# Optimization experiments

Hardware: AMD Instinct MI355X
Metric: run time of the kernel (lower is better)

The kernel has to match this reference:

```python
import jax, jax.numpy as jnp
import numpy as np
import math

B, T, C = 2, 2048, 1024
H = 16
D = C // H            # head_dim = 64
E = 4                 # num_experts
TOP_K = 1
EPS_RMS = 1.1920929e-07  # torch fp32 machine eps (F.rms_norm default)


def rms_norm(x):
    # F.rms_norm over last dim, no learned weight
    ms = jnp.mean(jnp.square(x), axis=-1, keepdims=True)
    return x * jax.lax.rsqrt(ms + EPS_RMS)


def rotary_cos_sin(seq_len, dim):
    inv_freq = 1.0 / (10000.0 ** (jnp.arange(0, dim, 2, dtype=jnp.float32) / dim))
    t = jnp.arange(seq_len, dtype=jnp.float32)
    freqs = jnp.outer(t, inv_freq)                 # [T, D/2]
    return jnp.cos(freqs)[None, :, None, :], jnp.sin(freqs)[None, :, None, :]


def apply_rotary(x, cos, sin):
    d = x.shape[-1] // 2
    x1, x2 = x[..., :d], x[..., d:]
    return jnp.concatenate([x1 * cos + x2 * sin, -x1 * sin + x2 * cos], axis=-1)


def setup_inputs() -> dict:
    key = jax.random.key(0)
    ks = jax.random.split(key, 8)
    s_attn = 1.0 / math.sqrt(C)
    s_fc = 1.0 / math.sqrt(C)
    s_pr = 1.0 / math.sqrt(4 * C)
    return {
        "x": jax.random.normal(ks[0], (B, T, C), jnp.float32),
        "Wq": jax.random.normal(ks[1], (C, C), jnp.float32) * s_attn,
        "Wk": jax.random.normal(ks[2], (C, C), jnp.float32) * s_attn,
        "Wv": jax.random.normal(ks[3], (C, C), jnp.float32) * s_attn,
        "Wo": jax.random.normal(ks[4], (C, C), jnp.float32) * s_attn,
        "Wr": jax.random.normal(ks[5], (C, E), jnp.float32) * s_attn,
        "Wfc": jax.random.normal(ks[6], (E, C, 4 * C), jnp.float32) * s_fc,
        "Wproj": jax.random.normal(ks[7], (E, 4 * C, C), jnp.float32) * s_pr,
    }


def attention(x, Wq, Wk, Wv, Wo):
    h = rms_norm(x)
    q = (h @ Wq).reshape(B, T, H, D)
    k = (h @ Wk).reshape(B, T, H, D)
    v = (h @ Wv).reshape(B, T, H, D)
    cos, sin = rotary_cos_sin(T, D)
    q, k = rms_norm(q), rms_norm(k)
    q, k = apply_rotary(q, cos, sin), apply_rotary(k, cos, sin)
    # causal SDPA, scale 1/sqrt(D)
    scores = jnp.einsum("bqhd,bkhd->bhqk", q, k) / math.sqrt(D)
    causal = jnp.tril(jnp.ones((T, T), dtype=bool))
    scores = jnp.where(causal, scores, jnp.finfo(scores.dtype).min)
    attn = jax.nn.softmax(scores, axis=-1)
    y = jnp.einsum("bhqk,bkhd->bqhd", attn, v).reshape(B, T, C)
    return y @ Wo


def moe(h, Wr, Wfc, Wproj):
    logits = h @ Wr                                # [B,T,E]
    probs = jax.nn.softmax(logits, axis=-1)
    gate, topk_idx = jax.lax.top_k(probs, TOP_K)   # [B,T,K]
    gate = gate / (jnp.sum(gate, axis=-1, keepdims=True) + 0.0)
    # expert mixing: top_k=1 -> per-token one expert. E=4 is tiny, so run
    # each expert densely and combine with the gate mask (same math as
    # the torch gather/index_add loop).
    y = jnp.zeros_like(h)
    for e in range(E):
        w_e = jnp.sum(jnp.where(topk_idx == e, gate, 0.0), axis=-1, keepdims=True)  # [B,T,1]
        hid = jnp.square(jax.nn.relu(h @ Wfc[e]))
        y = y + w_e * (hid @ Wproj[e])
    # router entropy (no-grad in torch)
    p = jax.lax.stop_gradient(probs.reshape(-1, E))
    token_H = -jnp.sum(p * jnp.log(p + 1e-09), axis=-1)
    router_entropy = jnp.mean(token_H) / math.log(float(E))
    # aux load-balance loss
    counts = jnp.bincount(topk_idx.reshape(-1), length=E).astype(jnp.float32)
    actual = counts / jnp.sum(counts)
    expected = jnp.mean(probs.reshape(-1, E), axis=0)
    aux = E * jnp.sum(actual * expected)
    # router z-loss
    z_loss = jnp.mean(jax.nn.logsumexp(logits, axis=-1) ** 2.0)
    return y, aux, z_loss, router_entropy, actual


def reference(x, Wq, Wk, Wv, Wo, Wr, Wfc, Wproj):
    x = x + attention(x, Wq, Wk, Wv, Wo)
    mlp_out, aux, z_loss, ent, frac = moe(rms_norm(x), Wr, Wfc, Wproj)
    x = x + mlp_out
    return (x, aux, z_loss, ent, frac)
```

## Files before the change

kernel.cpp:

```cpp
#include <hip/hip_runtime.h>
#include <stdint.h>

typedef unsigned short u16;
typedef __attribute__((ext_vector_type(8))) __bf16 bf16x8;
typedef __attribute__((ext_vector_type(4))) float f32x4;

#define T_SEQ 2048
#define CDIM 1024
#define NH 16
#define HD 64
#define NTOK 4096
#define EPS_RMS 1.1920929e-07f
#define LDKs 72
#define BSWZ(n, kk) ((kk) ^ ((((n) >> 2) & 7) << 3))

__device__ __forceinline__ u16 f2bf(float x) {
  union { float f; uint32_t u; } v; v.f = x;
  uint32_t r = v.u + 0x7fffu + ((v.u >> 16) & 1u);
  return (u16)(r >> 16);
}
__device__ __forceinline__ float bf2f(u16 h) {
  union { uint32_t u; float f; } v; v.u = ((uint32_t)h) << 16; return v.f;
}
__device__ __forceinline__ bf16x8 ld8(const u16* p) {
  uint4 q = *(const uint4*)p;
  return __builtin_bit_cast(bf16x8, q);
}
#define MFMA16(a, b, c) __builtin_amdgcn_mfma_f32_16x16x32_bf16((a), (b), (c), 0, 0, 0)

__global__ __launch_bounds__(256) void rope_table_k(float* __restrict__ cosT, float* __restrict__ sinT) {
  int idx = blockIdx.x * 256 + threadIdx.x;
  int t = idx >> 5, d = idx & 31;
  float inv = 1.0f / powf(10000.0f, (float)(2 * d) / 64.0f);
  float a = (float)t * inv;
  cosT[idx] = cosf(a);
  sinT[idx] = sinf(a);
}

__global__ __launch_bounds__(256) void rmsnorm_f_k(const float* __restrict__ x, float* __restrict__ hf) {
  int row = blockIdx.x;
  const float* xr = x + (size_t)row * CDIM;
  int tid = threadIdx.x;
  float v[4]; float s = 0.f;
  for (int i = 0; i < 4; ++i) { v[i] = xr[tid + 256 * i]; s += v[i] * v[i]; }
  for (int off = 32; off >= 1; off >>= 1) s += __shfl_xor(s, off);
  __shared__ float red[4];
  int w = tid >> 6, lane = tid & 63;
  if (lane == 0) red[w] = s;
  __syncthreads();
  s = red[0] + red[1] + red[2] + red[3];
  float rs = 1.0f / sqrtf(s * (1.f / CDIM) + EPS_RMS);
  for (int i = 0; i < 4; ++i) hf[(size_t)row * CDIM + tid + 256 * i] = v[i] * rs;
}

__global__ __launch_bounds__(256) void rmsnorm_b_k(const float* __restrict__ x, u16* __restrict__ hb) {
  int row = blockIdx.x;
  const float* xr = x + (size_t)row * CDIM;
  int tid = threadIdx.x;
  float v[4]; float s = 0.f;
  for (int i = 0; i < 4; ++i) { v[i] = xr[tid + 256 * i]; s += v[i] * v[i]; }
  for (int off = 32; off >= 1; off >>= 1) s += __shfl_xor(s, off);
  __shared__ float red[4];
  int w = tid >> 6, lane = tid & 63;
  if (lane == 0) red[w] = s;
  __syncthreads();
  s = red[0] + red[1] + red[2] + red[3];
  float rs = 1.0f / sqrtf(s * (1.f / CDIM) + EPS_RMS);
  for (int i = 0; i < 4; ++i) hb[(size_t)row * CDIM + tid + 256 * i] = f2bf(v[i] * rs);
}

template <int EPI>
__global__ __launch_bounds__(256) void gemm_split_k(const float* __restrict__ A, const float* __restrict__ B,
                                                    const float* __restrict__ Xadd, float* __restrict__ outF,
                                                    u16* __restrict__ outH, u16* __restrict__ outL,
                                                    const float* __restrict__ cosT, const float* __restrict__ sinT) {
  const int N = CDIM, K = CDIM;
  __shared__ __align__(16) u16 Ah[128][LDKs];
  __shared__ __align__(16) u16 Al[128][LDKs];
  __shared__ __align__(16) u16 Bh[128][LDKs];
  __shared__ __align__(16) u16 Bl[128][LDKs];
  int m0 = blockIdx.y * 128, n0 = blockIdx.x * 128;
  int tid = threadIdx.x, lane = tid & 63, w = tid >> 6;
  int wr = w >> 1, wc = w & 1;
  int fr = lane & 15, fq = lane >> 4, kof = fq * 8;
  f32x4 acc[4][4] = {};
  for (int kt = 0; kt < K; kt += 64) {
    #pragma unroll
    for (int i = 0; i < 8; ++i) {
      int slot = tid + i * 256;
      int r = slot >> 4, q = slot & 15;
      float4 v = *(const float4*)(A + (size_t)(m0 + r) * K + kt + q * 4);
      ushort4 hi, lo;
      hi.x = f2bf(v.x); lo.x = f2bf(v.x - bf2f(hi.x));
      hi.y = f2bf(v.y); lo.y = f2bf(v.y - bf2f(hi.y));
      hi.z = f2bf(v.z); lo.z = f2bf(v.z - bf2f(hi.z));
      hi.w = f2bf(v.w); lo.w = f2bf(v.w - bf2f(hi.w));
      *(ushort4*)&Ah[r][q * 4] = hi;
      *(ushort4*)&Al[r][q * 4] = lo;
    }
    #pragma unroll
    for (int i = 0; i < 2; ++i) {
      int sub = tid + i * 256;
      int nb = (sub & 31) * 4;
      int kk0 = (sub >> 5) * 4;
      float4 r0 = *(const float4*)(B + (size_t)(kt + kk0 + 0) * N + n0 + nb);
      float4 r1 = *(const float4*)(B + (size_t)(kt + kk0 + 1) * N + n0 + nb);
      float4 r2 = *(const float4*)(B + (size_t)(kt + kk0 + 2) * N + n0 + nb);
      float4 r3 = *(const float4*)(B + (size_t)(kt + kk0 + 3) * N + n0 + nb);
      float cv[4][4] = {{r0.x, r1.x, r2.x, r3.x}, {r0.y, r1.y, r2.y, r3.y},
                        {r0.z, r1.z, r2.z, r3.z}, {r0.w, r1.w, r2.w, r3.w}};
      #pragma unroll
      for (int c = 0; c < 4; ++c) {
        int n = nb + c;
        int kp = BSWZ(n, kk0);
        ushort4 hi, lo;
        hi.x = f2bf(cv[c][0]); lo.x = f2bf(cv[c][0] - bf2f(hi.x));
        hi.y = f2bf(cv[c][1]); lo.y = f2bf(cv[c][1] - bf2f(hi.y));
        hi.z = f2bf(cv[c][2]); lo.z = f2bf(cv[c][2] - bf2f(hi.z));
        hi.w = f2bf(cv[c][3]); lo.w = f2bf(cv[c][3] - bf2f(hi.w));
        *(ushort4*)&Bh[n][kp] = hi;
        *(ushort4*)&Bl[n][kp] = lo;
      }
    }
    __syncthreads();
    #pragma unroll
    for (int ks = 0; ks < 2; ++ks) {
      int kk = ks * 32 + kof;
      bf16x8 ah[4], al[4], bh4[4], bl4[4];
      #pragma unroll
      for (int i = 0; i < 4; ++i) {
        ah[i] = ld8(&Ah[wr * 64 + i * 16 + fr][kk]);
        al[i] = ld8(&Al[wr * 64 + i * 16 + fr][kk]);
      }
      #pragma unroll
      for (int j = 0; j < 4; ++j) {
        int n = wc * 64 + j * 16 + fr;
        bh4[j] = ld8(&Bh[n][BSWZ(n, kk)]);
        bl4[j] = ld8(&Bl[n][BSWZ(n, kk)]);
      }
      #pragma unroll
      for (int i = 0; i < 4; ++i)
        #pragma unroll
        for (int j = 0; j < 4; ++j) {
          acc[i][j] = MFMA16(al[i], bh4[j], acc[i][j]);
          acc[i][j] = MFMA16(ah[i], bl4[j], acc[i][j]);
          acc[i][j] = MFMA16(ah[i], bh4[j], acc[i][j]);
        }
    }
    __syncthreads();
  }
  if (EPI == 0) {
    int h = (n0 + wc * 64) >> 6;
    #pragma unroll
    for (int i = 0; i < 4; ++i) {
      #pragma unroll
      for (int j = 0; j < 4; ++j) {
        int row = m0 + wr * 64 + i * 16 + fq * 4 + j;
        float v0 = acc[i][0][j], v1 = acc[i][1][j], v2 = acc[i][2][j], v3 = acc[i][3][j];
        float ss = v0 * v0 + v1 * v1 + v2 * v2 + v3 * v3;
        ss += __shfl_xor(ss, 1); ss += __shfl_xor(ss, 2);
        ss += __shfl_xor(ss, 4); ss += __shfl_xor(ss, 8);
        float rs = 1.0f / sqrtf(ss * (1.f / HD) + EPS_RMS);
        float x0 = v0 * rs, x1 = v1 * rs, x2 = v2 * rs, x3 = v3 * rs;
        int t = row & (T_SEQ - 1), b = row >> 11;
        float c0 = cosT[t * 32 + fr],      s0 = sinT[t * 32 + fr];
        float c1 = cosT[t * 32 + fr + 16], s1 = sinT[t * 32 + fr + 16];
        float o0 = x0 * c0 + x2 * s0;
        float o1 = x1 * c1 + x3 * s1;
        float o2 = x2 * c0 - x0 * s0;
        float o3 = x3 * c1 - x1 * s1;
        size_t base = ((size_t)(b * NH + h) * T_SEQ + t) * HD + fr;
        u16 hh;
        hh = f2bf(o0); outH[base]      = hh; outL[base]      = f2bf(o0 - bf2f(hh));
        hh = f2bf(o1); outH[base + 16] = hh; outL[base + 16] = f2bf(o1 - bf2f(hh));
        hh = f2bf(o2); outH[base + 32] = hh; outL[base + 32] = f2bf(o2 - bf2f(hh));
        hh = f2bf(o3); outH[base + 48] = hh; outL[base + 48] = f2bf(o3 - bf2f(hh));
      }
    }
  } else {
    #pragma unroll
    for (int i = 0; i < 4; ++i)
      #pragma unroll
      for (int j = 0; j < 4; ++j) {
        int row = m0 + wr * 64 + i * 16 + fq * 4 + j;
        #pragma unroll
        for (int jf = 0; jf < 4; ++jf) {
          int gn = n0 + wc * 64 + jf * 16 + fr;
          float v = acc[i][jf][j];
          if (EPI == 1) {
            u16 hh = f2bf(v);
            outH[(size_t)row * CDIM + gn] = hh;
            outL[(size_t)row * CDIM + gn] = f2bf(v - bf2f(hh));
          } else {
            outF[(size_t)row * CDIM + gn] = Xadd[(size_t)row * CDIM + gn] + v;
          }
        }
      }
  }
}

__global__ __launch_bounds__(256) void vtrans_k(const u16* __restrict__ vhp, const u16* __restrict__ vlp,
                                                u16* __restrict__ vthp, u16* __restrict__ vtlp) {
  const u16* src = blockIdx.z ? vlp : vhp;
  u16* dst = blockIdx.z ? vtlp : vthp;
  __shared__ u16 t_[64][65];
  int bh = blockIdx.y, b = bh >> 4, h = bh & 15;
  int t0 = blockIdx.x * 64;
  const u16* in = src + ((size_t)b * T_SEQ) * CDIM + (size_t)h * HD;
  u16* out = dst + (size_t)bh * HD * T_SEQ;
  int tx = threadIdx.x & 63, ty = threadIdx.x >> 6;
  for (int i = ty; i < 64; i += 4) t_[i][tx] = in[(size_t)(t0 + i) * CDIM + tx];
  __syncthreads();
  for (int i = ty; i < 64; i += 4) out[(size_t)i * T_SEQ + t0 + tx] = t_[tx][i];
}

__global__ __launch_bounds__(64) void attn_k(const u16* __restrict__ qhp, const u16* __restrict__ qlp,
                                             const u16* __restrict__ khp, const u16* __restrict__ klp,
                                             const u16* __restrict__ vth, const u16* __restrict__ vtl,
                                             float* __restrict__ y) {
  int bh = blockIdx.y, qt = blockIdx.x;
  int lane = threadIdx.x;
  size_t o1 = (size_t)bh * T_SEQ * HD;
  const u16* Qh = qhp + o1; const u16* Ql = qlp + o1;
  const u16* Kh = khp + o1; const u16* Kl = klp + o1;
  const u16* Vh = vth + o1; const u16* Vl = vtl + o1;
  int q0 = qt * 32;
  int l15 = lane & 15, lg = lane >> 4, kof = lg * 8;
  bf16x8 aqh[2][2], aql[2][2];
  for (int m = 0; m < 2; ++m)
    for (int kc = 0; kc < 2; ++kc) {
      size_t p = (size_t)(q0 + 16 * m + l15) * HD + kc * 32 + kof;
      aqh[m][kc] = ld8(Qh + p);
      aql[m][kc] = ld8(Ql + p);
    }
  f32x4 o[2][4] = {};
  float mrow[2][4], lrow[2][4];
  for (int m = 0; m < 2; ++m)
    for (int r = 0; r < 4; ++r) { mrow[m][r] = -1e30f; lrow[m][r] = 0.f; }
  __shared__ __align__(16) float P_s[32][36];
  for (int j = 0; j <= qt; ++j) {
    int t0 = j * 32;
    bf16x8 bkh[2][2], bkl[2][2];
    for (int n = 0; n < 2; ++n)
      for (int kc = 0; kc < 2; ++kc) {
        size_t p = (size_t)(t0 + 16 * n + l15) * HD + kc * 32 + kof;
        bkh[n][kc] = ld8(Kh + p);
        bkl[n][kc] = ld8(Kl + p);
      }
    f32x4 sfr[2][2];
    for (int m = 0; m < 2; ++m)
      for (int n = 0; n < 2; ++n) {
        f32x4 z = {};
        for (int kc = 0; kc < 2; ++kc) {
          z = MFMA16(aql[m][kc], bkh[n][kc], z);
          z = MFMA16(aqh[m][kc], bkl[n][kc], z);
          z = MFMA16(aqh[m][kc], bkh[n][kc], z);
        }
        sfr[m][n] = z;
      }
    for (int m = 0; m < 2; ++m) {
      for (int r = 0; r < 4; ++r) {
        int grow = q0 + 16 * m + lg * 4 + r;
        float v0 = sfr[m][0][r] * 0.125f;
        float v1 = sfr[m][1][r] * 0.125f;
        if (t0 + l15 > grow) v0 = -1e30f;
        if (t0 + 16 + l15 > grow) v1 = -1e30f;
        float mx = fmaxf(v0, v1);
        for (int off = 8; off >= 1; off >>= 1) mx = fmaxf(mx, __shfl_xor(mx, off));
        float mnew = fmaxf(mrow[m][r], mx);
        float alpha = __expf(mrow[m][r] - mnew);
        float p0 = __expf(v0 - mnew);
        float p1 = __expf(v1 - mnew);
        float ps = p0 + p1;
        for (int off = 8; off >= 1; off >>= 1) ps += __shfl_xor(ps, off);
        mrow[m][r] = mnew;
        lrow[m][r] = lrow[m][r] * alpha + ps;
        for (int dt = 0; dt < 4; ++dt) o[m][dt][r] *= alpha;
        P_s[16 * m + lg * 4 + r][l15] = p0;
        P_s[16 * m + lg * 4 + r][l15 + 16] = p1;
      }
    }
    __syncthreads();
    bf16x8 ph[2], pl[2];
    for (int m = 0; m < 2; ++m)
      for (int jj = 0; jj < 8; ++jj) {
        float vv = P_s[16 * m + l15][kof + jj];
        u16 hv = f2bf(vv);
        ph[m][jj] = __builtin_bit_cast(__bf16, hv);
        pl[m][jj] = __builtin_bit_cast(__bf16, f2bf(vv - bf2f(hv)));
      }
    __syncthreads();
    for (int m = 0; m < 2; ++m)
      for (int dt = 0; dt < 4; ++dt) {
        size_t vp = (size_t)(dt * 16 + l15) * T_SEQ + t0 + kof;
        bf16x8 bvh = ld8(Vh + vp);
        bf16x8 bvl = ld8(Vl + vp);
        o[m][dt] = MFMA16(pl[m], bvh, o[m][dt]);
        o[m][dt] = MFMA16(ph[m], bvl, o[m][dt]);
        o[m][dt] = MFMA16(ph[m], bvh, o[m][dt]);
      }
  }
  int b = bh >> 4, h = bh & 15;
  for (int m = 0; m < 2; ++m)
    for (int r = 0; r < 4; ++r) {
      float inv = 1.f / lrow[m][r];
      int grow = q0 + 16 * m + lg * 4 + r;
      for (int dt = 0; dt < 4; ++dt)
        y[((size_t)b * T_SEQ + grow) * CDIM + h * HD + dt * 16 + l15] = o[m][dt][r] * inv;
    }
}

template <int MODE>
__global__ __launch_bounds__(256) void gemm_moe_k(const u16* __restrict__ Abf, const float* __restrict__ Ball,
                                                  void* __restrict__ Cout, const float* __restrict__ Xadd,
                                                  const int* __restrict__ perm, const int* __restrict__ cnt,
                                                  const int* __restrict__ offs) {
  const int N = (MODE == 0) ? 4096 : 1024;
  const int K = (MODE == 0) ? 1024 : 4096;
  int e = blockIdx.z;
  int Me = cnt[e];
  int m0 = blockIdx.y * 128;
  if (m0 >= Me) return;
  int n0 = blockIdx.x * 128;
  int offE = offs[e];
  const int* permE = perm + offE;
  const float* B = Ball + (size_t)e * (size_t)K * (size_t)N;
  __shared__ __align__(16) u16 As[128][LDKs];
  __shared__ __align__(16) u16 Bs[128][LDKs];
  int tid = threadIdx.x, lane = tid & 63, w = tid >> 6;
  int wr = w >> 1, wc = w & 1;
  int fr = lane & 15, fq = lane >> 4, kof = fq * 8;
  f32x4 acc[4][4] = {};
  for (int kt = 0; kt < K; kt += 64) {
    #pragma unroll
    for (int i = 0; i < 4; ++i) {
      int slot = tid + i * 256;
      int r = slot >> 3, col = (slot & 7) * 8;
      const u16* src;
      if (MODE == 0) {
        int gr = m0 + r;
        int tok = permE[gr < Me ? gr : 0];
        src = Abf + (size_t)tok * K + kt + col;
      } else {
        int gr = m0 + r; if (gr >= Me) gr = Me - 1;
        src = Abf + (size_t)(offE + gr) * K + kt + col;
      }
      *(uint4*)&As[r][col] = *(const uint4*)src;
    }
    #pragma unroll
    for (int i = 0; i < 2; ++i) {
      int sub = tid + i * 256;
      int nb = (sub & 31) * 4;
      int kk0 = (sub >> 5) * 4;
      float4 r0 = *(const float4*)(B + (size_t)(kt + kk0 + 0) * N + n0 + nb);
      float4 r1 = *(const float4*)(B + (size_t)(kt + kk0 + 1) * N + n0 + nb);
      float4 r2 = *(const float4*)(B + (size_t)(kt + kk0 + 2) * N + n0 + nb);
      float4 r3 = *(const float4*)(B + (size_t)(kt + kk0 + 3) * N + n0 + nb);
      float cv[4][4] = {{r0.x, r1.x, r2.x, r3.x}, {r0.y, r1.y, r2.y, r3.y},
                        {r0.z, r1.z, r2.z, r3.z}, {r0.w, r1.w, r2.w, r3.w}};
      #pragma unroll
      for (int c = 0; c < 4; ++c) {
        int n = nb + c;
        int kp = BSWZ(n, kk0);
        ushort4 hi;
        hi.x = f2bf(cv[c][0]); hi.y = f2bf(cv[c][1]);
        hi.z = f2bf(cv[c][2]); hi.w = f2bf(cv[c][3]);
        *(ushort4*)&Bs[n][kp] = hi;
      }
    }
    __syncthreads();
    #pragma unroll
    for (int ks = 0; ks < 2; ++ks) {
      int kk = ks * 32 + kof;
      bf16x8 af[4], bfr[4];
      #pragma unroll
      for (int i = 0; i < 4; ++i) af[i] = ld8(&As[wr * 64 + i * 16 + fr][kk]);
      #pragma unroll
      for (int j = 0; j < 4; ++j) {
        int n = wc * 64 + j * 16 + fr;
        bfr[j] = ld8(&Bs[n][BSWZ(n, kk)]);
      }
      #pragma unroll
      for (int i = 0; i < 4; ++i)
        #pragma unroll
        for (int j = 0; j < 4; ++j)
          acc[i][j] = MFMA16(af[i], bfr[j], acc[i][j]);
    }
    __syncthreads();
  }
  #pragma unroll
  for (int i = 0; i < 4; ++i)
    #pragma unroll
    for (int j = 0; j < 4; ++j) {
      int lrow = wr * 64 + i * 16 + fq * 4 + j;
      int gm = m0 + lrow;
      if (gm >= Me) continue;
      #pragma unroll
      for (int jf = 0; jf < 4; ++jf) {
        int gn = n0 + wc * 64 + jf * 16 + fr;
        float v = acc[i][jf][j];
        if (MODE == 0) {
          float rv = fmaxf(v, 0.f);
          ((u16*)Cout)[(size_t)(offE + gm) * N + gn] = f2bf(rv * rv);
        } else {
          int tok = permE[gm];
          ((float*)Cout)[(size_t)tok * N + gn] = Xadd[(size_t)tok * N + gn] + v;
        }
      }
    }
}

__global__ __launch_bounds__(64) void router_k(const float* __restrict__ xnew, const float* __restrict__ Wr,
                                               int* __restrict__ eidx, int* __restrict__ cnt,
                                               float* __restrict__ ts) {
  int t = blockIdx.x, lane = threadIdx.x;
  const float* h = xnew + (size_t)t * CDIM;
  float a0 = 0, a1 = 0, a2 = 0, a3 = 0, ss = 0;
  for (int i = lane; i < CDIM; i += 64) {
    float hv = h[i];
    ss += hv * hv;
    float4 wr = ((const float4*)Wr)[i];
    a0 += hv * wr.x; a1 += hv * wr.y; a2 += hv * wr.z; a3 += hv * wr.w;
  }
  for (int off = 32; off >= 1; off >>= 1) {
    a0 += __shfl_xor(a0, off); a1 += __shfl_xor(a1, off);
    a2 += __shfl_xor(a2, off); a3 += __shfl_xor(a3, off);
    ss += __shfl_xor(ss, off);
  }
  if (lane == 0) {
    float rs = 1.0f / sqrtf(ss * (1.f / CDIM) + EPS_RMS);
    float l[4] = {a0 * rs, a1 * rs, a2 * rs, a3 * rs};
    int am = 0; float mx = l[0];
    for (int e = 1; e < 4; ++e) if (l[e] > mx) { mx = l[e]; am = e; }
    float p[4], sum = 0;
    for (int e = 0; e < 4; ++e) { p[e] = __expf(l[e] - mx); sum += p[e]; }
    float lse = mx + logf(sum);
    float H = 0;
    for (int e = 0; e < 4; ++e) {
      float pr = p[e] / sum;
      H -= pr * logf(pr + 1e-9f);
      ts[t * 8 + e] = pr;
    }
    ts[t * 8 + 4] = H;
    ts[t * 8 + 5] = lse * lse;
    atomicAdd(&cnt[am], 1);
    eidx[t] = am;
  }
}

__global__ __launch_bounds__(256) void reduce_k(const float* __restrict__ ts, const int* __restrict__ cnt,
                                                int* __restrict__ offs, int* __restrict__ cursor,
                                                float* __restrict__ outs) {
  __shared__ float buf[6][256];
  int tid = threadIdx.x;
  float s[6] = {0, 0, 0, 0, 0, 0};
  for (int t = tid; t < NTOK; t += 256)
    for (int k = 0; k < 6; ++k) s[k] += ts[t * 8 + k];
  for (int k = 0; k < 6; ++k) buf[k][tid] = s[k];
  __syncthreads();
  for (int st = 128; st >= 1; st >>= 1) {
    if (tid < st)
      for (int k = 0; k < 6; ++k) buf[k][tid] += buf[k][tid + st];
    __syncthreads();
  }
  if (tid == 0) {
    int o = 0;
    for (int e = 0; e < 4; ++e) { offs[e] = o; o += cnt[e]; cursor[e] = 0; }
    float aux = 0;
    for (int e = 0; e < 4; ++e)
      aux += ((float)cnt[e] * (1.f / NTOK)) * (buf[e][0] * (1.f / NTOK));
    outs[0] = 4.f * aux;
    outs[1] = buf[5][0] * (1.f / NTOK);
    outs[2] = (buf[4][0] * (1.f / NTOK)) / logf(4.f);
    for (int e = 0; e < 4; ++e) outs[3 + e] = (float)cnt[e] * (1.f / NTOK);
  }
}

__global__ __launch_bounds__(256) void scatter_k(const int* __restrict__ eidx, const int* __restrict__ offs,
                                                 int* __restrict__ cursor, int* __restrict__ perm) {
  int t = blockIdx.x * 256 + threadIdx.x;
  if (t >= NTOK) return;
  int e = eidx[t];
  int pos = atomicAdd(&cursor[e], 1);
  perm[offs[e] + pos] = t;
}

extern "C" void kernel_launch(void* const* d_in, const int* in_sizes, int n_in,
                              void* d_out, int out_size, void* d_ws, size_t ws_size,
                              hipStream_t stream) {
  (void)in_sizes; (void)n_in; (void)out_size; (void)ws_size;
  const float* x   = (const float*)d_in[0];
  const float* Wq  = (const float*)d_in[1];
  const float* Wk  = (const float*)d_in[2];
  const float* Wv  = (const float*)d_in[3];
  const float* Wo  = (const float*)d_in[4];
  const float* Wr  = (const float*)d_in[5];
  const float* Wfc = (const float*)d_in[6];
  const float* Wpr = (const float*)d_in[7];
  float* out = (float*)d_out;
  uint8_t* ws = (uint8_t*)d_ws;

  size_t off = 0;
  auto alloc = [&](size_t b) { size_t p = off; off += (b + 255) & ~(size_t)255; return p; };
  float* ropeC = (float*)(ws + alloc(262144));
  float* ropeS = (float*)(ws + alloc(262144));
  float* ts    = (float*)(ws + alloc(131072));
  int* eidx = (int*)(ws + alloc(16384));
  int* perm = (int*)(ws + alloc(16384));
  uint8_t* stats = ws + alloc(256);
  int* cnt = (int*)stats;
  int* offsv = cnt + 4;
  int* cursor = cnt + 8;
  float* h1  = (float*)(ws + alloc(16777216));
  u16* qh = (u16*)(ws + alloc(8388608));
  u16* ql = (u16*)(ws + alloc(8388608));
  u16* kh = (u16*)(ws + alloc(8388608));
  u16* kl = (u16*)(ws + alloc(8388608));
  u16* vh = (u16*)(ws + alloc(8388608));
  u16* vl = (u16*)(ws + alloc(8388608));
  u16* vth = (u16*)(ws + alloc(8388608));
  u16* vtl = (u16*)(ws + alloc(8388608));
  float* xnew = h1;
  float* yb   = (float*)vh;
  u16* h2b    = kh;
  u16* hid    = vh;

  hipMemsetAsync(stats, 0, 256, stream);
  rope_table_k<<<256, 256, 0, stream>>>(ropeC, ropeS);
  rmsnorm_f_k<<<NTOK, 256, 0, stream>>>(x, h1);

  gemm_split_k<0><<<dim3(8, 32), 256, 0, stream>>>(h1, Wq, nullptr, nullptr, qh, ql, ropeC, ropeS);
  gemm_split_k<0><<<dim3(8, 32), 256, 0, stream>>>(h1, Wk, nullptr, nullptr, kh, kl, ropeC, ropeS);
  gemm_split_k<1><<<dim3(8, 32), 256, 0, stream>>>(h1, Wv, nullptr, nullptr, vh, vl, nullptr, nullptr);
  vtrans_k<<<dim3(32, 32, 2), 256, 0, stream>>>(vh, vl, vth, vtl);
  attn_k<<<dim3(64, 32), 64, 0, stream>>>(qh, ql, kh, kl, vth, vtl, yb);
  gemm_split_k<2><<<dim3(8, 32), 256, 0, stream>>>(yb, Wo, x, xnew, nullptr, nullptr, nullptr, nullptr);

  rmsnorm_b_k<<<NTOK, 256, 0, stream>>>(xnew, h2b);
  router_k<<<NTOK, 64, 0, stream>>>(xnew, Wr, eidx, cnt, ts);
  reduce_k<<<1, 256, 0, stream>>>(ts, cnt, offsv, cursor, out + 4194304);
  scatter_k<<<16, 256, 0, stream>>>(eidx, offsv, cursor, perm);
  gemm_moe_k<0><<<dim3(32, 32, 4), 256, 0, stream>>>(h2b, Wfc, hid, nullptr, perm, cnt, offsv);
  gemm_moe_k<1><<<dim3(8, 32, 4), 256, 0, stream>>>(hid, Wpr, out, xnew, perm, cnt, offsv);
}
```

Measured before the change: 1.061 ms.

## Pre-split and pre-transpose weights and activations to bf16 before GEMMs

Adds pre-pass kernels that convert the fp32 weights to transposed bf16 (hi/lo pairs for the attention projections, plain bf16 for the MoE experts). RMSNorm and attention now write bf16 hi/lo outputs directly, so the GEMM tile loaders become plain 16-byte copies with no per-tile conversion, transposition or swizzle. The conversion runs once per weight element rather than once per output tile that reads it. In exchange the extra passes cost memory traffic, and the shared-memory B tiles lose their XOR swizzle, which may bring back LDS bank conflicts.

After: 1.020 ms. 1.04x faster.

```diff
diff --git a/kernel.cpp b/kernel.cpp
--- a/kernel.cpp
+++ b/kernel.cpp
@@ -12,7 +12,6 @@
 #define NTOK 4096
 #define EPS_RMS 1.1920929e-07f
 #define LDKs 72
-#define BSWZ(n, kk) ((kk) ^ ((((n) >> 2) & 7) << 3))
 
 __device__ __forceinline__ u16 f2bf(float x) {
   union { float f; uint32_t u; } v; v.f = x;
@@ -37,7 +36,39 @@
   sinT[idx] = sinf(a);
 }
 
-__global__ __launch_bounds__(256) void rmsnorm_f_k(const float* __restrict__ x, float* __restrict__ hf) {
+__global__ __launch_bounds__(256) void wsplit_k(const float* __restrict__ in,
+                                                u16* __restrict__ ohi, u16* __restrict__ olo,
+                                                int R, int Cc) {
+  __shared__ float tile[32][33];
+  int c0 = blockIdx.x * 32, r0 = blockIdx.y * 32;
+  int tx = threadIdx.x & 31, ty = threadIdx.x >> 5;
+  for (int i = ty; i < 32; i += 8)
+    tile[i][tx] = in[(size_t)(r0 + i) * Cc + (c0 + tx)];
+  __syncthreads();
+  for (int i = ty; i < 32; i += 8) {
+    float v = tile[tx][i];
+    u16 h = f2bf(v);
+    ohi[(size_t)(c0 + i) * R + (r0 + tx)] = h;
+    olo[(size_t)(c0 + i) * R + (r0 + tx)] = f2bf(v - bf2f(h));
+  }
+}
+
+__global__ __launch_bounds__(256) void wcast_k(const float* __restrict__ in,
+                                               u16* __restrict__ out, int R, int Cc) {
+  size_t zoff = (size_t)blockIdx.z * (size_t)R * (size_t)Cc;
+  in += zoff; out += zoff;
+  __shared__ float tile[32][33];
+  int c0 = blockIdx.x * 32, r0 = blockIdx.y * 32;
+  int tx = threadIdx.x & 31, ty = threadIdx.x >> 5;
+  for (int i = ty; i < 32; i += 8)
+    tile[i][tx] = in[(size_t)(r0 + i) * Cc + (c0 + tx)];
+  __syncthreads();
+  for (int i = ty; i < 32; i += 8)
+    out[(size_t)(c0 + i) * R + (r0 + tx)] = f2bf(tile[tx][i]);
+}
+
+__global__ __launch_bounds__(256) void rmsnorm_split_k(const float* __restrict__ x,
+                                                       u16* __restrict__ hh, u16* __restrict__ hl) {
   int row = blockIdx.x;
   const float* xr = x + (size_t)row * CDIM;
   int tid = threadIdx.x;
@@ -50,7 +81,12 @@
   __syncthreads();
   s = red[0] + red[1] + red[2] + red[3];
   float rs = 1.0f / sqrtf(s * (1.f / CDIM) + EPS_RMS);
-  for (int i = 0; i < 4; ++i) hf[(size_t)row * CDIM + tid + 256 * i] = v[i] * rs;
+  for (int i = 0; i < 4; ++i) {
+    float o = v[i] * rs;
+    u16 h = f2bf(o);
+    hh[(size_t)row * CDIM + tid + 256 * i] = h;
+    hl[(size_t)row * CDIM + tid + 256 * i] = f2bf(o - bf2f(h));
+  }
 }
 
 __global__ __launch_bounds__(256) void rmsnorm_b_k(const float* __restrict__ x, u16* __restrict__ hb) {
@@ -70,10 +106,11 @@
 }
 
 template <int EPI>
-__global__ __launch_bounds__(256) void gemm_split_k(const float* __restrict__ A, const float* __restrict__ B,
-                                                    const float* __restrict__ Xadd, float* __restrict__ outF,
-                                                    u16* __restrict__ outH, u16* __restrict__ outL,
-                                                    const float* __restrict__ cosT, const float* __restrict__ sinT) {
+__global__ __launch_bounds__(256) void gemm_sp_k(const u16* __restrict__ Ahp, const u16* __restrict__ Alp,
+                                                 const u16* __restrict__ Bhp, const u16* __restrict__ Blp,
+                                                 const float* __restrict__ Xadd, float* __restrict__ outF,
+                                                 u16* __restrict__ outH, u16* __restrict__ outL,
+                                                 const float* __restrict__ cosT, const float* __restrict__ sinT) {
   const int N = CDIM, K = CDIM;
   __shared__ __align__(16) u16 Ah[128][LDKs];
   __shared__ __align__(16) u16 Al[128][LDKs];
@@ -83,44 +120,16 @@
   int tid = threadIdx.x, lane = tid & 63, w = tid >> 6;
   int wr = w >> 1, wc = w & 1;
   int fr = lane & 15, fq = lane >> 4, kof = fq * 8;
+  int rB = tid >> 3, colB = (tid & 7) * 8;
   f32x4 acc[4][4] = {};
   for (int kt = 0; kt < K; kt += 64) {
     #pragma unroll
-    for (int i = 0; i < 8; ++i) {
-      int slot = tid + i * 256;
-      int r = slot >> 4, q = slot & 15;
-      float4 v = *(const float4*)(A + (size_t)(m0 + r) * K + kt + q * 4);
-      ushort4 hi, lo;
-      hi.x = f2bf(v.x); lo.x = f2bf(v.x - bf2f(hi.x));
-      hi.y = f2bf(v.y); lo.y = f2bf(v.y - bf2f(hi.y));
-      hi.z = f2bf(v.z); lo.z = f2bf(v.z - bf2f(hi.z));
-      hi.w = f2bf(v.w); lo.w = f2bf(v.w - bf2f(hi.w));
-      *(ushort4*)&Ah[r][q * 4] = hi;
-      *(ushort4*)&Al[r][q * 4] = lo;
-    }
-    #pragma unroll
-    for (int i = 0; i < 2; ++i) {
-      int sub = tid + i * 256;
-      int nb = (sub & 31) * 4;
-      int kk0 = (sub >> 5) * 4;
-      float4 r0 = *(const float4*)(B + (size_t)(kt + kk0 + 0) * N + n0 + nb);
-      float4 r1 = *(const float4*)(B + (size_t)(kt + kk0 + 1) * N + n0 + nb);
-      float4 r2 = *(const float4*)(B + (size_t)(kt + kk0 + 2) * N + n0 + nb);
-      float4 r3 = *(const float4*)(B + (size_t)(kt + kk0 + 3) * N + n0 + nb);
-      float cv[4][4] = {{r0.x, r1.x, r2.x, r3.x}, {r0.y, r1.y, r2.y, r3.y},
-                        {r0.z, r1.z, r2.z, r3.z}, {r0.w, r1.w, r2.w, r3.w}};
-      #pragma unroll
-      for (int c = 0; c < 4; ++c) {
-        int n = nb + c;
-        int kp = BSWZ(n, kk0);
-        ushort4 hi, lo;
-        hi.x = f2bf(cv[c][0]); lo.x = f2bf(cv[c][0] - bf2f(hi.x));
-        hi.y = f2bf(cv[c][1]); lo.y = f2bf(cv[c][1] - bf2f(hi.y));
-        hi.z = f2bf(cv[c][2]); lo.z = f2bf(cv[c][2] - bf2f(hi.z));
-        hi.w = f2bf(cv[c][3]); lo.w = f2bf(cv[c][3] - bf2f(hi.w));
-        *(ushort4*)&Bh[n][kp] = hi;
-        *(ushort4*)&Bl[n][kp] = lo;
-      }
+    for (int i = 0; i < 4; ++i) {
+      int r = rB + i * 32;
+      *(uint4*)&Ah[r][colB] = *(const uint4*)(Ahp + (size_t)(m0 + r) * K + kt + colB);
+      *(uint4*)&Al[r][colB] = *(const uint4*)(Alp + (size_t)(m0 + r) * K + kt + colB);
+      *(uint4*)&Bh[r][colB] = *(const uint4*)(Bhp + (size_t)(n0 + r) * K + kt + colB);
+      *(uint4*)&Bl[r][colB] = *(const uint4*)(Blp + (size_t)(n0 + r) * K + kt + colB);
     }
     __syncthreads();
     #pragma unroll
@@ -134,9 +143,8 @@
       }
       #pragma unroll
       for (int j = 0; j < 4; ++j) {
-        int n = wc * 64 + j * 16 + fr;
-        bh4[j] = ld8(&Bh[n][BSWZ(n, kk)]);
-        bl4[j] = ld8(&Bl[n][BSWZ(n, kk)]);
+        bh4[j] = ld8(&Bh[wc * 64 + j * 16 + fr][kk]);
+        bl4[j] = ld8(&Bl[wc * 64 + j * 16 + fr][kk]);
       }
       #pragma unroll
       for (int i = 0; i < 4; ++i)
@@ -217,7 +225,7 @@
 __global__ __launch_bounds__(64) void attn_k(const u16* __restrict__ qhp, const u16* __restrict__ qlp,
                                              const u16* __restrict__ khp, const u16* __restrict__ klp,
                                              const u16* __restrict__ vth, const u16* __restrict__ vtl,
-                                             float* __restrict__ y) {
+                                             u16* __restrict__ yh, u16* __restrict__ yl) {
   int bh = blockIdx.y, qt = blockIdx.x;
   int lane = threadIdx.x;
   size_t o1 = (size_t)bh * T_SEQ * HD;
@@ -305,13 +313,18 @@
     for (int r = 0; r < 4; ++r) {
       float inv = 1.f / lrow[m][r];
       int grow = q0 + 16 * m + lg * 4 + r;
-      for (int dt = 0; dt < 4; ++dt)
-        y[((size_t)b * T_SEQ + grow) * CDIM + h * HD + dt * 16 + l15] = o[m][dt][r] * inv;
+      for (int dt = 0; dt < 4; ++dt) {
+        size_t idx = ((size_t)b * T_SEQ + grow) * CDIM + h * HD + dt * 16 + l15;
+        float vv = o[m][dt][r] * inv;
+        u16 hh = f2bf(vv);
+        yh[idx] = hh;
+        yl[idx] = f2bf(vv - bf2f(hh));
+      }
     }
 }
 
 template <int MODE>
-__global__ __launch_bounds__(256) void gemm_moe_k(const u16* __restrict__ Abf, const float* __restrict__ Ball,
+__global__ __launch_bounds__(256) void gemm_moe_k(const u16* __restrict__ Abf, const u16* __restrict__ BT,
                                                   void* __restrict__ Cout, const float* __restrict__ Xadd,
                                                   const int* __restrict__ perm, const int* __restrict__ cnt,
                                                   const int* __restrict__ offs) {
@@ -324,49 +337,32 @@
   int n0 = blockIdx.x * 128;
   int offE = offs[e];
   const int* permE = perm + offE;
-  const float* B = Ball + (size_t)e * (size_t)K * (size_t)N;
+  const u16* BTe = BT + (size_t)e * (size_t)N * (size_t)K;
   __shared__ __align__(16) u16 As[128][LDKs];
   __shared__ __align__(16) u16 Bs[128][LDKs];
   int tid = threadIdx.x, lane = tid & 63, w = tid >> 6;
   int wr = w >> 1, wc = w & 1;
   int fr = lane & 15, fq = lane >> 4, kof = fq * 8;
+  int rB = tid >> 3, colB = (tid & 7) * 8;
+  const u16* asrc[4];
+  #pragma unroll
+  for (int i = 0; i < 4; ++i) {
+    int gr = m0 + rB + i * 32;
+    if (MODE == 0) {
+      int tok = permE[gr < Me ? gr : 0];
+      asrc[i] = Abf + (size_t)tok * K;
+    } else {
+      if (gr >= Me) gr = Me - 1;
+      asrc[i] = Abf + (size_t)(offE + gr) * K;
+    }
+  }
   f32x4 acc[4][4] = {};
   for (int kt = 0; kt < K; kt += 64) {
     #pragma unroll
     for (int i = 0; i < 4; ++i) {
-      int slot = tid + i * 256;
-      int r = slot >> 3, col = (slot & 7) * 8;
-      const u16* src;
-      if (MODE == 0) {
-        int gr = m0 + r;
-        int tok = permE[gr < Me ? gr : 0];
-        src = Abf + (size_t)tok * K + kt + col;
-      } else {
-        int gr = m0 + r; if (gr >= Me) gr = Me - 1;
-        src = Abf + (size_t)(offE + gr) * K + kt + col;
-      }
-      *(uint4*)&As[r][col] = *(const uint4*)src;
-    }
-    #pragma unroll
-    for (int i = 0; i < 2; ++i) {
-      int sub = tid + i * 256;
-      int nb = (sub & 31) * 4;
-      int kk0 = (sub >> 5) * 4;
-      float4 r0 = *(const float4*)(B + (size_t)(kt + kk0 + 0) * N + n0 + nb);
-      float4 r1 = *(const float4*)(B + (size_t)(kt + kk0 + 1) * N + n0 + nb);
-      float4 r2 = *(const float4*)(B + (size_t)(kt + kk0 + 2) * N + n0 + nb);
-      float4 r3 = *(const float4*)(B + (size_t)(kt + kk0 + 3) * N + n0 + nb);
-      float cv[4][4] = {{r0.x, r1.x, r2.x, r3.x}, {r0.y, r1.y, r2.y, r3.y},
-                        {r0.z, r1.z, r2.z, r3.z}, {r0.w, r1.w, r2.w, r3.w}};
-      #pragma unroll
-      for (int c = 0; c < 4; ++c) {
-        int n = nb + c;
-        int kp = BSWZ(n, kk0);
-        ushort4 hi;
-        hi.x = f2bf(cv[c][0]); hi.y = f2bf(cv[c][1]);
-        hi.z = f2bf(cv[c][2]); hi.w = f2bf(cv[c][3]);
-        *(ushort4*)&Bs[n][kp] = hi;
-      }
+      int r = rB + i * 32;
+      *(uint4*)&As[r][colB] = *(const uint4*)(asrc[i] + kt + colB);
+      *(uint4*)&Bs[r][colB] = *(const uint4*)(BTe + (size_t)(n0 + r) * K + kt + colB);
     }
     __syncthreads();
     #pragma unroll
@@ -376,10 +372,7 @@
       #pragma unroll
       for (int i = 0; i < 4; ++i) af[i] = ld8(&As[wr * 64 + i * 16 + fr][kk]);
       #pragma unroll
-      for (int j = 0; j < 4; ++j) {
-        int n = wc * 64 + j * 16 + fr;
-        bfr[j] = ld8(&Bs[n][BSWZ(n, kk)]);
-      }
+      for (int j = 0; j < 4; ++j) bfr[j] = ld8(&Bs[wc * 64 + j * 16 + fr][kk]);
       #pragma unroll
       for (int i = 0; i < 4; ++i)
         #pragma unroll
@@ -511,7 +504,17 @@
   int* cnt = (int*)stats;
   int* offsv = cnt + 4;
   int* cursor = cnt + 8;
-  float* h1  = (float*)(ws + alloc(16777216));
+  u16* wqh = (u16*)(ws + alloc(2097152));
+  u16* wql = (u16*)(ws + alloc(2097152));
+  u16* wkh = (u16*)(ws + alloc(2097152));
+  u16* wkl = (u16*)(ws + alloc(2097152));
+  u16* wvh = (u16*)(ws + alloc(2097152));
+  u16* wvl = (u16*)(ws + alloc(2097152));
+  u16* woh = (u16*)(ws + alloc(2097152));
+  u16* wol = (u16*)(ws + alloc(2097152));
+  u16* wfcT = (u16*)(ws + alloc(33554432));
+  u16* h1h = (u16*)(ws + alloc(8388608));
+  u16* h1l = (u16*)(ws + alloc(8388608));
   u16* qh = (u16*)(ws + alloc(8388608));
   u16* ql = (u16*)(ws + alloc(8388608));
   u16* kh = (u16*)(ws + alloc(8388608));
@@ -520,26 +523,34 @@
   u16* vl = (u16*)(ws + alloc(8388608));
   u16* vth = (u16*)(ws + alloc(8388608));
   u16* vtl = (u16*)(ws + alloc(8388608));
-  float* xnew = h1;
-  float* yb   = (float*)vh;
-  u16* h2b    = kh;
-  u16* hid    = vh;
+  float* xnew = (float*)h1h;
+  u16* yh = vh;
+  u16* yl = vl;
+  u16* h2b = vth;
+  u16* hid = qh;
+  u16* wprT = wfcT;
 
   hipMemsetAsync(stats, 0, 256, stream);
   rope_table_k<<<256, 256, 0, stream>>>(ropeC, ropeS);
-  rmsnorm_f_k<<<NTOK, 256, 0, stream>>>(x, h1);
-
-  gemm_split_k<0><<<dim3(8, 32), 256, 0, stream>>>(h1, Wq, nullptr, nullptr, qh, ql, ropeC, ropeS);
-  gemm_split_k<0><<<dim3(8, 32), 256, 0, stream>>>(h1, Wk, nullptr, nullptr, kh, kl, ropeC, ropeS);
-  gemm_split_k<1><<<dim3(8, 32), 256, 0, stream>>>(h1, Wv, nullptr, nullptr, vh, vl, nullptr, nullptr);
+  wsplit_k<<<dim3(32, 32), 256, 0, stream>>>(Wq, wqh, wql, 1024, 1024);
+  wsplit_k<<<dim3(32, 32), 256, 0, stream>>>(Wk, wkh, wkl, 1024, 1024);
+  wsplit_k<<<dim3(32, 32), 256, 0, stream>>>(Wv, wvh, wvl, 1024, 1024);
+  wsplit_k<<<dim3(32, 32), 256, 0, stream>>>(Wo, woh, wol, 1024, 1024);
+  wcast_k<<<dim3(128, 32, 4), 256, 0, stream>>>(Wfc, wfcT, 1024, 4096);
+  rmsnorm_split_k<<<NTOK, 256, 0, stream>>>(x, h1h, h1l);
+
+  gemm_sp_k<0><<<dim3(8, 32), 256, 0, stream>>>(h1h, h1l, wqh, wql, nullptr, nullptr, qh, ql, ropeC, ropeS);
+  gemm_sp_k<0><<<dim3(8, 32), 256, 0, stream>>>(h1h, h1l, wkh, wkl, nullptr, nullptr, kh, kl, ropeC, ropeS);
+  gemm_sp_k<1><<<dim3(8, 32), 256, 0, stream>>>(h1h, h1l, wvh, wvl, nullptr, nullptr, vh, vl, nullptr, nullptr);
   vtrans_k<<<dim3(32, 32, 2), 256, 0, stream>>>(vh, vl, vth, vtl);
-  attn_k<<<dim3(64, 32), 64, 0, stream>>>(qh, ql, kh, kl, vth, vtl, yb);
-  gemm_split_k<2><<<dim3(8, 32), 256, 0, stream>>>(yb, Wo, x, xnew, nullptr, nullptr, nullptr, nullptr);
+  attn_k<<<dim3(64, 32), 64, 0, stream>>>(qh, ql, kh, kl, vth, vtl, yh, yl);
+  gemm_sp_k<2><<<dim3(8, 32), 256, 0, stream>>>(yh, yl, woh, wol, x, xnew, nullptr, nullptr, nullptr, nullptr);
 
   rmsnorm_b_k<<<NTOK, 256, 0, stream>>>(xnew, h2b);
   router_k<<<NTOK, 64, 0, stream>>>(xnew, Wr, eidx, cnt, ts);
   reduce_k<<<1, 256, 0, stream>>>(ts, cnt, offsv, cursor, out + 4194304);
   scatter_k<<<16, 256, 0, stream>>>(eidx, offsv, cursor, perm);
-  gemm_moe_k<0><<<dim3(32, 32, 4), 256, 0, stream>>>(h2b, Wfc, hid, nullptr, perm, cnt, offsv);
-  gemm_moe_k<1><<<dim3(8, 32, 4), 256, 0, stream>>>(hid, Wpr, out, xnew, perm, cnt, offsv);
-}
+  gemm_moe_k<0><<<dim3(32, 32, 4), 256, 0, stream>>>(h2b, wfcT, hid, nullptr, perm, cnt, offsv);
+  wcast_k<<<dim3(32, 128, 4), 256, 0, stream>>>(Wpr, wprT, 4096, 1024);
+  gemm_moe_k<1><<<dim3(8, 32, 4), 256, 0, stream>>>(hid, wprT, out, xnew, perm, cnt, offsv);
+}
```
